# Optimization experiments

Hardware: AMD Instinct MI355X
Metric: run time of the kernel (lower is better)

## Reference

```python
import jax, jax.numpy as jnp
import numpy as np

COST_MASK = 5.0
COST_DICE = 5.0
COST_BOX = 5.0
COST_GIOU = 2.0


def point_sample(masks, pts):
    # masks: [N, H, W]; pts: [P, 2] with (x, y) in [0, 1].
    # Matches F.grid_sample(bilinear, align_corners=False, padding_mode='zeros')
    N, H, W = masks.shape
    x = pts[:, 0] * W - 0.5
    y = pts[:, 1] * H - 0.5
    x0 = jnp.floor(x)
    y0 = jnp.floor(y)
    wx = x - x0
    wy = y - y0
    x0i = x0.astype(jnp.int32)
    y0i = y0.astype(jnp.int32)

    def gather(yi, xi):
        valid = ((xi >= 0) & (xi < W) & (yi >= 0) & (yi < H)).astype(masks.dtype)
        v = masks[:, jnp.clip(yi, 0, H - 1), jnp.clip(xi, 0, W - 1)]  # [N, P]
        return v * valid

    v00 = gather(y0i, x0i)
    v01 = gather(y0i, x0i + 1)
    v10 = gather(y0i + 1, x0i)
    v11 = gather(y0i + 1, x0i + 1)
    return (v00 * (1 - wy) * (1 - wx) + v01 * (1 - wy) * wx
            + v10 * wy * (1 - wx) + v11 * wy * wx)  # [N, P]


def box_cxcywh_to_xyxy(b):
    cx, cy, w, h = b[..., 0], b[..., 1], b[..., 2], b[..., 3]
    return jnp.stack([cx - 0.5 * w, cy - 0.5 * h, cx + 0.5 * w, cy + 0.5 * h], axis=-1)


def generalized_box_iou(a, b):
    # a: [Q, 4], b: [T, 4] in xyxy
    area_a = (a[:, 2] - a[:, 0]) * (a[:, 3] - a[:, 1])
    area_b = (b[:, 2] - b[:, 0]) * (b[:, 3] - b[:, 1])
    lt = jnp.maximum(a[:, None, :2], b[None, :, :2])
    rb = jnp.minimum(a[:, None, 2:], b[None, :, 2:])
    wh = jnp.clip(rb - lt, 0.0)
    inter = wh[..., 0] * wh[..., 1]
    union = area_a[:, None] + area_b[None, :] - inter
    iou = inter / union
    lt_e = jnp.minimum(a[:, None, :2], b[None, :, :2])
    rb_e = jnp.maximum(a[:, None, 2:], b[None, :, 2:])
    wh_e = jnp.clip(rb_e - lt_e, 0.0)
    area_e = wh_e[..., 0] * wh_e[..., 1]
    return iou - (area_e - union) / area_e


def _cost_one(out_mask, tgt_mask, out_box, tgt_box, pts):
    om = point_sample(out_mask, pts)  # [Q, P] logits
    tm = point_sample(tgt_mask, pts)  # [T, P] binary targets
    P = om.shape[1]
    # batch_sigmoid_ce_loss: BCE(x,1)=softplus(-x), BCE(x,0)=softplus(x)
    pos = jax.nn.softplus(-om)
    neg = jax.nn.softplus(om)
    cost_mask = (jnp.einsum('qp,tp->qt', pos, tm)
                 + jnp.einsum('qp,tp->qt', neg, 1.0 - tm)) / P
    # batch_dice_loss
    s = jax.nn.sigmoid(om)
    numerator = 2.0 * jnp.einsum('qp,tp->qt', s, tm)
    denominator = s.sum(-1)[:, None] + tm.sum(-1)[None, :]
    cost_dice = 1.0 - (numerator + 1.0) / (denominator + 1.0)
    # box costs
    cost_bbox = jnp.abs(out_box[:, None, :] - tgt_box[None, :, :]).sum(-1)
    cost_giou = -generalized_box_iou(box_cxcywh_to_xyxy(out_box),
                                     box_cxcywh_to_xyxy(tgt_box))
    return (COST_MASK * cost_mask + COST_DICE * cost_dice
            + COST_BOX * cost_bbox + COST_GIOU * cost_giou)


def setup_inputs() -> dict:
    key = jax.random.key(0)
    k1, k2, k3, k4, k5 = jax.random.split(key, 5)
    B, Q, T, H, W, P = 2, 300, 300, 256, 256, 12544
    pred_masks = jax.random.normal(k1, (B, Q, H, W), dtype=jnp.float32)
    tgt_masks = (jax.random.uniform(k2, (B, T, H, W)) > 0.5).astype(jnp.float32)
    u = jax.random.uniform(k3, (B, Q, 4), dtype=jnp.float32)
    pred_boxes = jnp.concatenate([0.2 + 0.6 * u[..., :2], 0.05 + 0.25 * u[..., 2:]], axis=-1)
    v = jax.random.uniform(k4, (B, T, 4), dtype=jnp.float32)
    tgt_boxes = jnp.concatenate([0.2 + 0.6 * v[..., :2], 0.05 + 0.25 * v[..., 2:]], axis=-1)
    point_coords = jax.random.uniform(k5, (B, P, 2), dtype=jnp.float32)
    return {"pred_masks": pred_masks, "tgt_masks": tgt_masks,
            "pred_boxes": pred_boxes, "tgt_boxes": tgt_boxes,
            "point_coords": point_coords}


def reference(pred_masks, tgt_masks, pred_boxes, tgt_boxes, point_coords):
    # Batched cost matrix C: [B, Q, T]
    return jax.vmap(_cost_one)(pred_masks, tgt_masks, pred_boxes, tgt_boxes, point_coords)
```

## Files before the change

kernel.cpp:

```cpp
#include <hip/hip_runtime.h>
#include <hip/hip_bf16.h>
#include <math.h>

#define BB 2
#define QQ 300
#define TT 300
#define HH 256
#define WW 256
#define PP 12544
#define NCHUNK 16
#define NSPLIT 14
#define KSPLIT (PP / NSPLIT)
#define KSTEPS (KSPLIT / 64)

typedef __bf16 bf16_t;
typedef bf16_t bf16x8 __attribute__((ext_vector_type(8)));
typedef float floatx4 __attribute__((ext_vector_type(4)));

__device__ inline void gl_lds16(const void* g, void* l) {
    __builtin_amdgcn_global_load_lds(
        (const __attribute__((address_space(1))) unsigned int*)g,
        (__attribute__((address_space(3))) unsigned int*)l, 16, 0, 0);
}

__global__ __launch_bounds__(256) void prep_kernel(const float* __restrict__ pts,
                                                   int4* __restrict__ off,
                                                   float4* __restrict__ wgt,
                                                   int* __restrict__ bkt) {
    int idx = blockIdx.x * 256 + threadIdx.x;
    if (idx >= BB * PP) return;
    float px = pts[idx * 2 + 0];
    float py = pts[idx * 2 + 1];
    float x = px * WW - 0.5f;
    float y = py * HH - 0.5f;
    float x0f = floorf(x), y0f = floorf(y);
    float wx = x - x0f, wy = y - y0f;
    int x0 = (int)x0f, y0 = (int)y0f;
    int x1 = x0 + 1, y1 = y0 + 1;
    float vx0 = (x0 >= 0 && x0 < WW) ? 1.f : 0.f;
    float vx1 = (x1 >= 0 && x1 < WW) ? 1.f : 0.f;
    float vy0 = (y0 >= 0 && y0 < HH) ? 1.f : 0.f;
    float vy1 = (y1 >= 0 && y1 < HH) ? 1.f : 0.f;
    int cx0 = min(max(x0, 0), WW - 1), cx1 = min(max(x1, 0), WW - 1);
    int cy0 = min(max(y0, 0), HH - 1), cy1 = min(max(y1, 0), HH - 1);
    off[idx] = make_int4(cy0 * WW + cx0, cy0 * WW + cx1, cy1 * WW + cx0, cy1 * WW + cx1);
    wgt[idx] = make_float4((1.f - wy) * (1.f - wx) * vy0 * vx0,
                           (1.f - wy) * wx        * vy0 * vx1,
                           wy        * (1.f - wx) * vy1 * vx0,
                           wy        * wx         * vy1 * vx1);
    bkt[idx] = min(max(y0, 0), HH - 2) >> 4;
}

__global__ __launch_bounds__(1024) void sort_kernel(const int4* __restrict__ off,
                                                    const float4* __restrict__ wgt,
                                                    const int* __restrict__ bkt,
                                                    int4* __restrict__ off_s,
                                                    float4* __restrict__ wgt_s,
                                                    int* __restrict__ cs) {
    int b = blockIdx.x;
    int tid = threadIdx.x;
    __shared__ int hist[NCHUNK];
    __shared__ int base_s[NCHUNK];
    if (tid < NCHUNK) hist[tid] = 0;
    __syncthreads();
    for (int p = tid; p < PP; p += 1024) atomicAdd(&hist[bkt[b * PP + p]], 1);
    __syncthreads();
    if (tid == 0) {
        int run = 0;
        for (int i = 0; i < NCHUNK; ++i) { base_s[i] = run; run += hist[i]; }
    }
    __syncthreads();
    if (tid < NCHUNK + 1) cs[b * (NCHUNK + 1) + tid] = (tid < NCHUNK) ? base_s[tid] : PP;
    __syncthreads();
    for (int p = tid; p < PP; p += 1024) {
        int bp = b * PP + p;
        int pos = atomicAdd(&base_s[bkt[bp]], 1);
        off_s[b * PP + pos] = off[bp];
        wgt_s[b * PP + pos] = wgt[bp];
    }
}

__global__ __launch_bounds__(256) void sample_kernel(
    const float* __restrict__ pred_masks, const float* __restrict__ tgt_masks,
    const int4* __restrict__ off_s, const float4* __restrict__ wgt_s,
    const int* __restrict__ cs_g,
    bf16_t* __restrict__ OM, bf16_t* __restrict__ SM, bf16_t* __restrict__ TM,
    float* __restrict__ RS_SP, float* __restrict__ RS_S, float* __restrict__ RS_T) {
    int b = blockIdx.z;
    int m = blockIdx.x;
    int c = blockIdx.y;
    int tid = threadIdx.x;
    int wave = tid >> 6, lane = tid & 63;
    __shared__ __align__(16) float rows[17 * WW];

    bool is_pred = (m < QQ);
    const float* img;
    bf16_t* row0;
    bf16_t* row1 = nullptr;
    if (is_pred) {
        img  = pred_masks + (size_t)(b * QQ + m) * (HH * WW);
        row0 = OM + (size_t)(b * QQ + m) * PP;
        row1 = SM + (size_t)(b * QQ + m) * PP;
    } else {
        int t = m - QQ;
        img  = tgt_masks + (size_t)(b * TT + t) * (HH * WW);
        row0 = TM + (size_t)(b * TT + t) * PP;
    }

    int base = c * 16;
    int nrows = min(17, HH - base);
    const char* gimg = (const char*)(img + base * WW);
    for (int i = wave; i < nrows; i += 4)
        gl_lds16(gimg + i * 1024 + lane * 16, (char*)rows + i * 1024);
    __syncthreads();

    const int4*  offb = off_s + b * PP;
    const float4* wb  = wgt_s + b * PP;
    const int* cs = cs_g + b * (NCHUNK + 1);
    int boff = base * WW;
    int j1 = cs[c + 1];
    float s0 = 0.f, s1 = 0.f;
    for (int j = cs[c] + tid; j < j1; j += 256) {
        int4 o = offb[j];
        float4 w = wb[j];
        float v = w.x * rows[o.x - boff] + w.y * rows[o.y - boff] +
                  w.z * rows[o.z - boff] + w.w * rows[o.w - boff];
        row0[j] = (bf16_t)v;
        if (is_pred) {
            float e = __expf(-fabsf(v));
            float r = 1.f / (1.f + e);
            float sg = (v >= 0.f) ? r : e * r;
            row1[j] = (bf16_t)sg;
            s0 += fmaxf(v, 0.f) + __logf(1.f + e);
            s1 += sg;
        } else {
            s0 += v;
        }
    }
    for (int o = 32; o > 0; o >>= 1) {
        s0 += __shfl_down(s0, o, 64);
        s1 += __shfl_down(s1, o, 64);
    }
    __shared__ float ra[4], rb[4];
    if (lane == 0) { ra[wave] = s0; rb[wave] = s1; }
    __syncthreads();
    if (tid == 0) {
        float t0 = ra[0] + ra[1] + ra[2] + ra[3];
        float t1 = rb[0] + rb[1] + rb[2] + rb[3];
        if (is_pred) {
            atomicAdd(&RS_SP[b * QQ + m], t0);
            atomicAdd(&RS_S[b * QQ + m], t1);
        } else {
            atomicAdd(&RS_T[b * TT + (m - QQ)], t0);
        }
    }
}

__global__ __launch_bounds__(256) void matmul_kernel(
    const bf16_t* __restrict__ OM, const bf16_t* __restrict__ SM, const bf16_t* __restrict__ TM,
    float* __restrict__ A1P, float* __restrict__ A2P) {
    int b = blockIdx.z / NSPLIT;
    int split = blockIdx.z % NSPLIT;
    int m0 = blockIdx.x * 64;
    int n0 = blockIdx.y * 64;
    int tid = threadIdx.x;
    int wave = tid >> 6, lane = tid & 63;
    int lrow = lane & 15, quad = lane >> 4;

    __shared__ __align__(16) bf16_t lds[3 * 64 * 64];

    int k0 = split * KSPLIT;
    int lr8 = lane >> 3;
    int clog = (lane & 7) ^ lr8;

    const char* gp[6];
    unsigned lofs[6];
#pragma unroll
    for (int jj = 0; jj < 6; ++jj) {
        int L = wave + jj * 4;
        int mat = L >> 3, i = L & 7;
        int rb_ = (mat == 2) ? n0 : m0;
        int row = min(rb_ + i * 8 + lr8, (mat == 2) ? (TT - 1) : (QQ - 1));
        const bf16_t* g = (mat == 0) ? OM + (size_t)b * QQ * PP
                        : (mat == 1) ? SM + (size_t)b * QQ * PP
                                     : TM + (size_t)b * TT * PP;
        gp[jj] = (const char*)(g + (size_t)row * PP + k0) + clog * 16;
        lofs[jj] = mat * 4096 + i * 512;
    }

    floatx4 acc1[4] = {{0.f,0.f,0.f,0.f},{0.f,0.f,0.f,0.f},{0.f,0.f,0.f,0.f},{0.f,0.f,0.f,0.f}};
    floatx4 acc2[4] = {{0.f,0.f,0.f,0.f},{0.f,0.f,0.f,0.f},{0.f,0.f,0.f,0.f},{0.f,0.f,0.f,0.f}};

    int ar = wave * 16 + lrow;
    int arx = ar & 7;
    for (int s = 0; s < KSTEPS; ++s) {
#pragma unroll
        for (int jj = 0; jj < 6; ++jj) {
            gl_lds16(gp[jj], lds + lofs[jj]);
            gp[jj] += 128;
        }
        __syncthreads();
#pragma unroll
        for (int kk8 = 0; kk8 <= 4; kk8 += 4) {
            bf16x8 a1 = *(const bf16x8*)(lds + ar * 64 + (((quad + kk8) ^ arx) << 3));
            bf16x8 a2 = *(const bf16x8*)(lds + 4096 + ar * 64 + (((quad + kk8) ^ arx) << 3));
#pragma unroll
            for (int j = 0; j < 4; ++j) {
                int br = j * 16 + lrow;
                bf16x8 bb = *(const bf16x8*)(lds + 8192 + br * 64 + (((quad + kk8) ^ (br & 7)) << 3));
                acc1[j] = __builtin_amdgcn_mfma_f32_16x16x32_bf16(a1, bb, acc1[j], 0, 0, 0);
                acc2[j] = __builtin_amdgcn_mfma_f32_16x16x32_bf16(a2, bb, acc2[j], 0, 0, 0);
            }
        }
        __syncthreads();
    }

    int mrow = m0 + wave * 16 + quad * 4;
    float* o1 = A1P + (size_t)(b * NSPLIT + split) * (QQ * TT);
    float* o2 = A2P + (size_t)(b * NSPLIT + split) * (QQ * TT);
#pragma unroll
    for (int j = 0; j < 4; ++j) {
        int n = n0 + j * 16 + lrow;
        if (n < TT) {
#pragma unroll
            for (int r = 0; r < 4; ++r) {
                int m = mrow + r;
                if (m < QQ) {
                    o1[m * TT + n] = acc1[j][r];
                    o2[m * TT + n] = acc2[j][r];
                }
            }
        }
    }
}

__global__ __launch_bounds__(256) void combine_kernel(
    const float* __restrict__ A1P, const float* __restrict__ A2P,
    const float* __restrict__ RS_SP, const float* __restrict__ RS_S, const float* __restrict__ RS_T,
    const float* __restrict__ pred_boxes, const float* __restrict__ tgt_boxes,
    float* __restrict__ out) {
    int idx = blockIdx.x * 256 + threadIdx.x;
    if (idx >= BB * QQ * TT) return;
    int b = idx / (QQ * TT);
    int r = idx - b * (QQ * TT);
    int q = r / TT;
    int t = r - q * TT;

    float a1 = 0.f, a2 = 0.f;
    for (int s = 0; s < NSPLIT; ++s) {
        a1 += A1P[(size_t)(b * NSPLIT + s) * (QQ * TT) + r];
        a2 += A2P[(size_t)(b * NSPLIT + s) * (QQ * TT) + r];
    }
    float cm = (RS_SP[b * QQ + q] - a1) * (1.0f / (float)PP);
    float cd = 1.f - (2.f * a2 + 1.f) / (RS_S[b * QQ + q] + RS_T[b * TT + t] + 1.f);

    const float* pb = pred_boxes + (size_t)(b * QQ + q) * 4;
    const float* tb = tgt_boxes + (size_t)(b * TT + t) * 4;
    float cb = fabsf(pb[0] - tb[0]) + fabsf(pb[1] - tb[1]) +
               fabsf(pb[2] - tb[2]) + fabsf(pb[3] - tb[3]);

    float ax0 = pb[0] - 0.5f * pb[2], ay0 = pb[1] - 0.5f * pb[3];
    float ax1 = pb[0] + 0.5f * pb[2], ay1 = pb[1] + 0.5f * pb[3];
    float bx0 = tb[0] - 0.5f * tb[2], by0 = tb[1] - 0.5f * tb[3];
    float bx1 = tb[0] + 0.5f * tb[2], by1 = tb[1] + 0.5f * tb[3];
    float area_a = (ax1 - ax0) * (ay1 - ay0);
    float area_b = (bx1 - bx0) * (by1 - by0);
    float iw = fmaxf(fminf(ax1, bx1) - fmaxf(ax0, bx0), 0.f);
    float ih = fmaxf(fminf(ay1, by1) - fmaxf(ay0, by0), 0.f);
    float inter = iw * ih;
    float uni = area_a + area_b - inter;
    float iou = inter / uni;
    float ew = fmaxf(ax1, bx1) - fminf(ax0, bx0);
    float eh = fmaxf(ay1, by1) - fminf(ay0, by0);
    float area_e = ew * eh;
    float giou = iou - (area_e - uni) / area_e;

    out[idx] = 5.f * cm + 5.f * cd + 5.f * cb - 2.f * giou;
}

extern "C" void kernel_launch(void* const* d_in, const int* in_sizes, int n_in,
                              void* d_out, int out_size, void* d_ws, size_t ws_size,
                              hipStream_t stream) {
    const float* pred_masks = (const float*)d_in[0];
    const float* tgt_masks  = (const float*)d_in[1];
    const float* pred_boxes = (const float*)d_in[2];
    const float* tgt_boxes  = (const float*)d_in[3];
    const float* pts        = (const float*)d_in[4];

    char* w = (char*)d_ws;
    auto alloc = [&](size_t bytes) -> char* {
        char* r = w;
        w += (bytes + 255) & ~(size_t)255;
        return r;
    };
    int4*   OFF   = (int4*)  alloc((size_t)BB * PP * sizeof(int4));
    float4* WGT   = (float4*)alloc((size_t)BB * PP * sizeof(float4));
    int*    BKT   = (int*)   alloc((size_t)BB * PP * sizeof(int));
    int4*   OFF_S = (int4*)  alloc((size_t)BB * PP * sizeof(int4));
    float4* WGT_S = (float4*)alloc((size_t)BB * PP * sizeof(float4));
    int*    CS    = (int*)   alloc((size_t)BB * (NCHUNK + 1) * sizeof(int));
    bf16_t* OM    = (bf16_t*)alloc((size_t)BB * QQ * PP * 2);
    bf16_t* SM    = (bf16_t*)alloc((size_t)BB * QQ * PP * 2);
    bf16_t* TM    = (bf16_t*)alloc((size_t)BB * TT * PP * 2);
    float*  RS_SP = (float*) alloc((size_t)BB * QQ * 4);
    float*  RS_S  = (float*) alloc((size_t)BB * QQ * 4);
    float*  RS_T  = (float*) alloc((size_t)BB * TT * 4);
    float*  A1P   = (float*) alloc((size_t)BB * NSPLIT * QQ * TT * 4);
    float*  A2P   = (float*) alloc((size_t)BB * NSPLIT * QQ * TT * 4);

    hipMemsetAsync(RS_SP, 0, (size_t)((char*)A1P - (char*)RS_SP), stream);

    prep_kernel<<<(BB * PP + 255) / 256, 256, 0, stream>>>(pts, OFF, WGT, BKT);
    sort_kernel<<<BB, 1024, 0, stream>>>(OFF, WGT, BKT, OFF_S, WGT_S, CS);
    sample_kernel<<<dim3(QQ + TT, NCHUNK, BB), 256, 0, stream>>>(
        pred_masks, tgt_masks, OFF_S, WGT_S, CS, OM, SM, TM, RS_SP, RS_S, RS_T);
    matmul_kernel<<<dim3(5, 5, BB * NSPLIT), 256, 0, stream>>>(OM, SM, TM, A1P, A2P);
    combine_kernel<<<(BB * QQ * TT + 255) / 256, 256, 0, stream>>>(
        A1P, A2P, RS_SP, RS_S, RS_T, pred_boxes, tgt_boxes, (float*)d_out);
}
```

Baseline: 395.6 us.

## Parallelize point bucketing and fuse pred/target sampling per block

Replaces the two-block sort kernel with a grid-wide histogram in prep, a tiny scan kernel, and a wave-aggregated atomic scatter kernel, so bucketing runs across many blocks. The sample kernel now handles one pred mask and one target mask per block, loading both row strips into LDS and reusing the same offsets and weights for both. The first few points per thread are prefetched before the barrier. This cuts the serial sort latency and halves offset/weight reads, at the cost of doubled LDS per block (lower occupancy), one extra launch, and nondeterministic point order within a bucket.

```diff
diff --git a/kernel.cpp b/kernel.cpp
--- a/kernel.cpp
+++ b/kernel.cpp
@@ -26,9 +26,10 @@
 __global__ __launch_bounds__(256) void prep_kernel(const float* __restrict__ pts,
                                                    int4* __restrict__ off,
                                                    float4* __restrict__ wgt,
-                                                   int* __restrict__ bkt) {
+                                                   int* __restrict__ bkt,
+                                                   int* __restrict__ hist) {
     int idx = blockIdx.x * 256 + threadIdx.x;
-    if (idx >= BB * PP) return;
+    int b = idx / PP;
     float px = pts[idx * 2 + 0];
     float py = pts[idx * 2 + 1];
     float x = px * WW - 0.5f;
@@ -48,36 +49,47 @@
                            (1.f - wy) * wx        * vy0 * vx1,
                            wy        * (1.f - wx) * vy1 * vx0,
                            wy        * wx         * vy1 * vx1);
-    bkt[idx] = min(max(y0, 0), HH - 2) >> 4;
-}
-
-__global__ __launch_bounds__(1024) void sort_kernel(const int4* __restrict__ off,
-                                                    const float4* __restrict__ wgt,
-                                                    const int* __restrict__ bkt,
-                                                    int4* __restrict__ off_s,
-                                                    float4* __restrict__ wgt_s,
-                                                    int* __restrict__ cs) {
-    int b = blockIdx.x;
-    int tid = threadIdx.x;
-    __shared__ int hist[NCHUNK];
-    __shared__ int base_s[NCHUNK];
-    if (tid < NCHUNK) hist[tid] = 0;
-    __syncthreads();
-    for (int p = tid; p < PP; p += 1024) atomicAdd(&hist[bkt[b * PP + p]], 1);
-    __syncthreads();
-    if (tid == 0) {
-        int run = 0;
-        for (int i = 0; i < NCHUNK; ++i) { base_s[i] = run; run += hist[i]; }
-    }
-    __syncthreads();
-    if (tid < NCHUNK + 1) cs[b * (NCHUNK + 1) + tid] = (tid < NCHUNK) ? base_s[tid] : PP;
-    __syncthreads();
-    for (int p = tid; p < PP; p += 1024) {
-        int bp = b * PP + p;
-        int pos = atomicAdd(&base_s[bkt[bp]], 1);
-        off_s[b * PP + pos] = off[bp];
-        wgt_s[b * PP + pos] = wgt[bp];
-    }
+    int c = min(max(y0, 0), HH - 2) >> 4;
+    bkt[idx] = c;
+    atomicAdd(&hist[b * NCHUNK + c], 1);
+}
+
+__global__ void scan_kernel(const int* __restrict__ hist,
+                            int* __restrict__ cs, int* __restrict__ gbase) {
+    int b = threadIdx.x;
+    if (b >= BB) return;
+    int run = 0;
+    for (int i = 0; i < NCHUNK; ++i) {
+        cs[b * (NCHUNK + 1) + i] = run;
+        gbase[b * NCHUNK + i] = run;
+        run += hist[b * NCHUNK + i];
+    }
+    cs[b * (NCHUNK + 1) + NCHUNK] = run;
+}
+
+__global__ __launch_bounds__(256) void scatter_kernel(const int4* __restrict__ off,
+                                                      const float4* __restrict__ wgt,
+                                                      const int* __restrict__ bkt,
+                                                      int* __restrict__ gbase,
+                                                      int4* __restrict__ off_s,
+                                                      float4* __restrict__ wgt_s) {
+    int idx = blockIdx.x * 256 + threadIdx.x;
+    int b = idx / PP;
+    int lane = threadIdx.x & 63;
+    int my = bkt[idx];
+    int pos = 0;
+    for (int c = 0; c < NCHUNK; ++c) {
+        bool active = (my == c);
+        unsigned long long mask = __ballot(active);
+        if (mask == 0ull) continue;
+        int leader = __ffsll((unsigned long long)mask) - 1;
+        int base_v = 0;
+        if (lane == leader) base_v = atomicAdd(&gbase[b * NCHUNK + c], (int)__popcll(mask));
+        base_v = __shfl(base_v, leader, 64);
+        if (active) pos = base_v + (int)__popcll(mask & (((unsigned long long)1 << lane) - 1ull));
+    }
+    off_s[(size_t)b * PP + pos] = off[idx];
+    wgt_s[(size_t)b * PP + pos] = wgt[idx];
 }
 
 __global__ __launch_bounds__(256) void sample_kernel(
@@ -91,68 +103,86 @@
     int c = blockIdx.y;
     int tid = threadIdx.x;
     int wave = tid >> 6, lane = tid & 63;
-    __shared__ __align__(16) float rows[17 * WW];
-
-    bool is_pred = (m < QQ);
-    const float* img;
-    bf16_t* row0;
-    bf16_t* row1 = nullptr;
-    if (is_pred) {
-        img  = pred_masks + (size_t)(b * QQ + m) * (HH * WW);
-        row0 = OM + (size_t)(b * QQ + m) * PP;
-        row1 = SM + (size_t)(b * QQ + m) * PP;
-    } else {
-        int t = m - QQ;
-        img  = tgt_masks + (size_t)(b * TT + t) * (HH * WW);
-        row0 = TM + (size_t)(b * TT + t) * PP;
-    }
+    __shared__ __align__(16) float rows[2 * 17 * WW];
+
+    const float* ip = pred_masks + (size_t)(b * QQ + m) * (HH * WW);
+    const float* it = tgt_masks  + (size_t)(b * TT + m) * (HH * WW);
+    bf16_t* rowO = OM + (size_t)(b * QQ + m) * PP;
+    bf16_t* rowS = SM + (size_t)(b * QQ + m) * PP;
+    bf16_t* rowT = TM + (size_t)(b * TT + m) * PP;
 
     int base = c * 16;
     int nrows = min(17, HH - base);
-    const char* gimg = (const char*)(img + base * WW);
-    for (int i = wave; i < nrows; i += 4)
-        gl_lds16(gimg + i * 1024 + lane * 16, (char*)rows + i * 1024);
+    const char* gp = (const char*)(ip + base * WW);
+    const char* gt = (const char*)(it + base * WW);
+    for (int i = wave; i < nrows; i += 4) {
+        gl_lds16(gp + i * 1024 + lane * 16, (char*)rows + i * 1024);
+        gl_lds16(gt + i * 1024 + lane * 16, (char*)rows + 17408 + i * 1024);
+    }
+
+    const int4*  offb = off_s + (size_t)b * PP;
+    const float4* wb  = wgt_s + (size_t)b * PP;
+    const int* cs = cs_g + b * (NCHUNK + 1);
+    int j0 = cs[c], j1 = cs[c + 1];
+    int4 o_r[4]; float4 w_r[4];
+    int np = 0;
+    for (int j = j0 + tid; j < j1 && np < 4; j += 256) {
+        o_r[np] = offb[j];
+        w_r[np] = wb[j];
+        ++np;
+    }
     __syncthreads();
 
-    const int4*  offb = off_s + b * PP;
-    const float4* wb  = wgt_s + b * PP;
-    const int* cs = cs_g + b * (NCHUNK + 1);
     int boff = base * WW;
-    int j1 = cs[c + 1];
-    float s0 = 0.f, s1 = 0.f;
-    for (int j = cs[c] + tid; j < j1; j += 256) {
+    float s0 = 0.f, s1 = 0.f, s2 = 0.f;
+    for (int i = 0; i < np; ++i) {
+        int j = j0 + tid + i * 256;
+        int4 o = o_r[i];
+        float4 w = w_r[i];
+        int ox = o.x - boff, oy = o.y - boff, oz = o.z - boff, ow = o.w - boff;
+        float v = w.x * rows[ox] + w.y * rows[oy] + w.z * rows[oz] + w.w * rows[ow];
+        float u = w.x * rows[4352 + ox] + w.y * rows[4352 + oy] +
+                  w.z * rows[4352 + oz] + w.w * rows[4352 + ow];
+        rowO[j] = (bf16_t)v;
+        float e = __expf(-fabsf(v));
+        float r = 1.f / (1.f + e);
+        float sg = (v >= 0.f) ? r : e * r;
+        rowS[j] = (bf16_t)sg;
+        s0 += fmaxf(v, 0.f) + __logf(1.f + e);
+        s1 += sg;
+        rowT[j] = (bf16_t)u;
+        s2 += u;
+    }
+    for (int j = j0 + tid + 4 * 256; j < j1; j += 256) {
         int4 o = offb[j];
         float4 w = wb[j];
-        float v = w.x * rows[o.x - boff] + w.y * rows[o.y - boff] +
-                  w.z * rows[o.z - boff] + w.w * rows[o.w - boff];
-        row0[j] = (bf16_t)v;
-        if (is_pred) {
-            float e = __expf(-fabsf(v));
-            float r = 1.f / (1.f + e);
-            float sg = (v >= 0.f) ? r : e * r;
-            row1[j] = (bf16_t)sg;
-            s0 += fmaxf(v, 0.f) + __logf(1.f + e);
-            s1 += sg;
-        } else {
-            s0 += v;
-        }
-    }
+        int ox = o.x - boff, oy = o.y - boff, oz = o.z - boff, ow = o.w - boff;
+        float v = w.x * rows[ox] + w.y * rows[oy] + w.z * rows[oz] + w.w * rows[ow];
+        float u = w.x * rows[4352 + ox] + w.y * rows[4352 + oy] +
+                  w.z * rows[4352 + oz] + w.w * rows[4352 + ow];
+        rowO[j] = (bf16_t)v;
+        float e = __expf(-fabsf(v));
+        float r = 1.f / (1.f + e);
+        float sg = (v >= 0.f) ? r : e * r;
+        rowS[j] = (bf16_t)sg;
+        s0 += fmaxf(v, 0.f) + __logf(1.f + e);
+        s1 += sg;
+        rowT[j] = (bf16_t)u;
+        s2 += u;
+    }
+
     for (int o = 32; o > 0; o >>= 1) {
         s0 += __shfl_down(s0, o, 64);
         s1 += __shfl_down(s1, o, 64);
-    }
-    __shared__ float ra[4], rb[4];
-    if (lane == 0) { ra[wave] = s0; rb[wave] = s1; }
+        s2 += __shfl_down(s2, o, 64);
+    }
+    __shared__ float ra[4], rb[4], rc[4];
+    if (lane == 0) { ra[wave] = s0; rb[wave] = s1; rc[wave] = s2; }
     __syncthreads();
     if (tid == 0) {
-        float t0 = ra[0] + ra[1] + ra[2] + ra[3];
-        float t1 = rb[0] + rb[1] + rb[2] + rb[3];
-        if (is_pred) {
-            atomicAdd(&RS_SP[b * QQ + m], t0);
-            atomicAdd(&RS_S[b * QQ + m], t1);
-        } else {
-            atomicAdd(&RS_T[b * TT + (m - QQ)], t0);
-        }
+        atomicAdd(&RS_SP[b * QQ + m], ra[0] + ra[1] + ra[2] + ra[3]);
+        atomicAdd(&RS_S [b * QQ + m], rb[0] + rb[1] + rb[2] + rb[3]);
+        atomicAdd(&RS_T [b * TT + m], rc[0] + rc[1] + rc[2] + rc[3]);
     }
 }
 
@@ -247,6 +277,7 @@
     int t = r - q * TT;
 
     float a1 = 0.f, a2 = 0.f;
+#pragma unroll
     for (int s = 0; s < NSPLIT; ++s) {
         a1 += A1P[(size_t)(b * NSPLIT + s) * (QQ * TT) + r];
         a2 += A2P[(size_t)(b * NSPLIT + s) * (QQ * TT) + r];
@@ -305,14 +336,17 @@
     float*  RS_SP = (float*) alloc((size_t)BB * QQ * 4);
     float*  RS_S  = (float*) alloc((size_t)BB * QQ * 4);
     float*  RS_T  = (float*) alloc((size_t)BB * TT * 4);
+    int*    HIST  = (int*)   alloc((size_t)BB * NCHUNK * sizeof(int));
+    int*    GBASE = (int*)   alloc((size_t)BB * NCHUNK * sizeof(int));
     float*  A1P   = (float*) alloc((size_t)BB * NSPLIT * QQ * TT * 4);
     float*  A2P   = (float*) alloc((size_t)BB * NSPLIT * QQ * TT * 4);
 
     hipMemsetAsync(RS_SP, 0, (size_t)((char*)A1P - (char*)RS_SP), stream);
 
-    prep_kernel<<<(BB * PP + 255) / 256, 256, 0, stream>>>(pts, OFF, WGT, BKT);
-    sort_kernel<<<BB, 1024, 0, stream>>>(OFF, WGT, BKT, OFF_S, WGT_S, CS);
-    sample_kernel<<<dim3(QQ + TT, NCHUNK, BB), 256, 0, stream>>>(
+    prep_kernel<<<(BB * PP) / 256, 256, 0, stream>>>(pts, OFF, WGT, BKT, HIST);
+    scan_kernel<<<1, 64, 0, stream>>>(HIST, CS, GBASE);
+    scatter_kernel<<<(BB * PP) / 256, 256, 0, stream>>>(OFF, WGT, BKT, GBASE, OFF_S, WGT_S);
+    sample_kernel<<<dim3(QQ, NCHUNK, BB), 256, 0, stream>>>(
         pred_masks, tgt_masks, OFF_S, WGT_S, CS, OM, SM, TM, RS_SP, RS_S, RS_T);
     matmul_kernel<<<dim3(5, 5, BB * NSPLIT), 256, 0, stream>>>(OM, SM, TM, A1P, A2P);
     combine_kernel<<<(BB * QQ * TT + 255) / 256, 256, 0, stream>>>(
```

Result: slower. 509.6 us (+28.8%).
